# Kernel tuning notes

Hardware: AMD Instinct MI355X
Metric: run time of the kernel (lower is better)

## Reference

```python
import jax, jax.numpy as jnp
import numpy as np

D_MODEL = 1024
NUM_HEADS = 16
GROUPS = 4
HEADS_PER_GROUP = NUM_HEADS // GROUPS
D_K = D_MODEL // NUM_HEADS
B, S = 2, 2048


def setup_inputs() -> dict:
    key = jax.random.key(0)
    ks = jax.random.split(key, 10)
    sc = 0.02
    return {
        "x": jax.random.normal(ks[0], (B, S, D_MODEL), dtype=jnp.float32),
        "W_Q": jax.random.normal(ks[1], (D_MODEL, D_MODEL), dtype=jnp.float32) * sc,
        "b_Q": jnp.zeros((D_MODEL,), dtype=jnp.float32),
        "W_K": jax.random.normal(ks[2], (GROUPS, D_MODEL, D_K), dtype=jnp.float32) * sc,
        "b_K": jnp.zeros((GROUPS, D_K), dtype=jnp.float32),
        "W_V": jax.random.normal(ks[3], (GROUPS, D_MODEL, D_K), dtype=jnp.float32) * sc,
        "b_V": jnp.zeros((GROUPS, D_K), dtype=jnp.float32),
        "W_O": jax.random.normal(ks[4], (D_MODEL, D_MODEL), dtype=jnp.float32) * sc,
        "b_O": jnp.zeros((D_MODEL,), dtype=jnp.float32),
    }


def reference(x, W_Q, b_Q, W_K, b_K, W_V, b_V, W_O, b_O):
    b, s, _ = x.shape
    # Q: [b, s, d_model] -> [b, groups, heads_per_group, s, d_k]
    Q = (x @ W_Q + b_Q).reshape(b, s, NUM_HEADS, D_K).transpose(0, 2, 1, 3)
    Q = Q.reshape(b, GROUPS, HEADS_PER_GROUP, s, D_K)
    # Shared K/V per group: [b, groups, s, d_k]
    K = jnp.einsum('bsd,gdk->bgsk', x, W_K) + b_K[None, :, None, :]
    V = jnp.einsum('bsd,gdk->bgsk', x, W_V) + b_V[None, :, None, :]
    # scores: [b, groups, heads_per_group, s, s]
    scores = jnp.einsum('bghsk,bgtk->bghst', Q, K) / jnp.sqrt(jnp.float32(D_K))
    attn = jax.nn.softmax(scores, axis=-1)
    # context: [b, groups, heads_per_group, s, d_k] -> [b, s, d_model]
    ctx = jnp.einsum('bghst,bgtk->bghsk', attn, V)
    ctx = ctx.reshape(b, NUM_HEADS, s, D_K).transpose(0, 2, 1, 3).reshape(b, s, D_MODEL)
    return ctx @ W_O + b_O
```

## Files before the change

kernel.cpp:

```cpp
#include <hip/hip_runtime.h>
#include <cstdint>
#include <cstddef>

typedef short bf16x8 __attribute__((ext_vector_type(8)));
typedef float f32x4 __attribute__((ext_vector_type(4)));

#define DM 1024
#define NHEADS 16
#define NGROUPS 4
#define DK 64
#define BATCH 2
#define SEQ 2048
#define MROWS 4096

#define QB_ELEMS   ((size_t)BATCH*NHEADS*SEQ*DK)
#define KB_ELEMS   ((size_t)BATCH*NGROUPS*SEQ*DK)
#define VT_ELEMS   KB_ELEMS
#define XC_ELEMS   ((size_t)MROWS*DM)
#define WQKV_ELEMS ((size_t)1536*DM)
#define WO_ELEMS   ((size_t)DM*DM)

__device__ __forceinline__ ushort f2bf(float f) {
    union { float f; uint32_t u; } a; a.f = f;
    uint32_t u = a.u;
    return (ushort)((u + 0x7FFFu + ((u >> 16) & 1u)) >> 16);
}
__device__ __forceinline__ ushort f2bf_rh(float f) {
    union { float f; uint32_t u; } a; a.f = f;
    return (ushort)((a.u + 0x8000u) >> 16);
}

__device__ __forceinline__ void gll16(const void* g, void* l) {
    __builtin_amdgcn_global_load_lds((const __attribute__((address_space(1))) void*)g,
                                     (__attribute__((address_space(3))) void*)l, 16, 0, 0);
}

__global__ __launch_bounds__(256) void gqa_prep_kernel(
        const float* __restrict__ x,
        const float* __restrict__ WQ, const float* __restrict__ WK,
        const float* __restrict__ WV, const float* __restrict__ WO,
        const float* __restrict__ bQ, const float* __restrict__ bK,
        const float* __restrict__ bV,
        ushort* __restrict__ xbf, ushort* __restrict__ WqkvT,
        ushort* __restrict__ WoT, float* __restrict__ bcat)
{
    __shared__ float tl[64][65];
    const int bid = blockIdx.x, tid = threadIdx.x;
    if (bid < 640) {
        const float* src; ushort* dst; int src_ld; int r0, c0;
        if (bid < 256) {
            src = WQ; src_ld = 1024; dst = WqkvT;
            r0 = (bid >> 4) * 64; c0 = (bid & 15) * 64;
        } else if (bid < 512) {
            int t = bid - 256;
            src = WO; src_ld = 1024; dst = WoT;
            r0 = (t >> 4) * 64; c0 = (t & 15) * 64;
        } else if (bid < 576) {
            int t = bid - 512; int g = t >> 4;
            src = WK + (size_t)g * 1024 * 64; src_ld = 64;
            dst = WqkvT + (size_t)(1024 + g * 64) * 1024;
            r0 = (t & 15) * 64; c0 = 0;
        } else {
            int t = bid - 576; int g = t >> 4;
            src = WV + (size_t)g * 1024 * 64; src_ld = 64;
            dst = WqkvT + (size_t)(1280 + g * 64) * 1024;
            r0 = (t & 15) * 64; c0 = 0;
        }
        const int rr = tid >> 4, cc = (tid & 15) * 4;
#pragma unroll
        for (int p = 0; p < 4; p++) {
            int r = rr + p * 16;
            float4 v = *(const float4*)(src + (size_t)(r0 + r) * src_ld + c0 + cc);
            tl[cc + 0][r] = v.x; tl[cc + 1][r] = v.y;
            tl[cc + 2][r] = v.z; tl[cc + 3][r] = v.w;
        }
        __syncthreads();
#pragma unroll
        for (int p = 0; p < 4; p++) {
            int c = rr + p * 16;
            ushort4 o;
            o.x = f2bf(tl[c][cc + 0]); o.y = f2bf(tl[c][cc + 1]);
            o.z = f2bf(tl[c][cc + 2]); o.w = f2bf(tl[c][cc + 3]);
            *(ushort4*)(dst + (size_t)(c0 + c) * 1024 + r0 + cc) = o;
        }
    } else if (bid < 896) {
        int cid = bid - 640;
        const float* xs = x + (size_t)cid * 16384;
        ushort* xd = xbf + (size_t)cid * 16384;
#pragma unroll
        for (int p = 0; p < 16; p++) {
            float4 v = *(const float4*)(xs + p * 1024 + tid * 4);
            ushort4 o = { f2bf(v.x), f2bf(v.y), f2bf(v.z), f2bf(v.w) };
            *(ushort4*)(xd + p * 1024 + tid * 4) = o;
        }
    } else {
        for (int i = tid; i < 1536; i += 256) {
            float v = (i < 1024) ? bQ[i] : (i < 1280 ? bK[i - 1024] : bV[i - 1280]);
            bcat[i] = v;
        }
    }
}

template<bool QKV_EPI>
__global__ __launch_bounds__(256, 2) void gqa_gemm_kernel(
        const ushort* __restrict__ A, const ushort* __restrict__ BT,
        const float* __restrict__ bias, float* __restrict__ outF,
        ushort* __restrict__ Qb, ushort* __restrict__ Kb, ushort* __restrict__ Vtg)
{
    __shared__ ushort As[2][128 * 32];
    __shared__ ushort Bs[2][64 * 32];
    const int tid = threadIdx.x;
    const int bm = blockIdx.x, bn = blockIdx.y;
    const int wave = tid >> 6, lane = tid & 63;
    const int wm = (wave & 1) * 64, wn = (wave >> 1) * 32;
    const int lr = lane & 15, lq = lane >> 4;

    const int sa0 = wave * 128 + lane;
    const int sa1 = sa0 + 64;
    const int sb0 = wave * 64 + lane;
    const ushort* srcA0 = A  + (size_t)(bm * 128 + (sa0 >> 2)) * 1024 + (sa0 & 3) * 8;
    const ushort* srcA1 = A  + (size_t)(bm * 128 + (sa1 >> 2)) * 1024 + (sa1 & 3) * 8;
    const ushort* srcB0 = BT + (size_t)(bn * 64  + (sb0 >> 2)) * 1024 + (sb0 & 3) * 8;

    f32x4 acc[4][2];
#pragma unroll
    for (int i = 0; i < 4; i++)
#pragma unroll
        for (int j = 0; j < 2; j++) acc[i][j] = (f32x4){0.f, 0.f, 0.f, 0.f};

    gll16(srcA0, &As[0][wave * 1024]);
    gll16(srcA1, &As[0][wave * 1024 + 512]);
    gll16(srcB0, &Bs[0][wave * 512]);

    for (int kt = 0; kt < 32; kt++) {
        __syncthreads();
        if (kt < 31) {
            int buf = (kt + 1) & 1, ko = (kt + 1) * 32;
            gll16(srcA0 + ko, &As[buf][wave * 1024]);
            gll16(srcA1 + ko, &As[buf][wave * 1024 + 512]);
            gll16(srcB0 + ko, &Bs[buf][wave * 512]);
        }
        const ushort* as = As[kt & 1];
        const ushort* bs = Bs[kt & 1];
        bf16x8 af[4], bfr[2];
#pragma unroll
        for (int i = 0; i < 4; i++) af[i]  = *(const bf16x8*)&as[(wm + i * 16 + lr) * 32 + lq * 8];
#pragma unroll
        for (int j = 0; j < 2; j++) bfr[j] = *(const bf16x8*)&bs[(wn + j * 16 + lr) * 32 + lq * 8];
#pragma unroll
        for (int i = 0; i < 4; i++)
#pragma unroll
            for (int j = 0; j < 2; j++)
                acc[i][j] = __builtin_amdgcn_mfma_f32_16x16x32_bf16(af[i], bfr[j], acc[i][j], 0, 0, 0);
    }

#pragma unroll
    for (int i = 0; i < 4; i++) {
        int mg = bm * 128 + wm + i * 16 + lq * 4;
        int b = mg >> 11, s = mg & 2047;
#pragma unroll
        for (int j = 0; j < 2; j++) {
            int cg = bn * 64 + wn + j * 16 + lr;
            float bv = bias[cg];
            if constexpr (QKV_EPI) {
                int d = cg & 63;
                if (cg < 1024) {
                    int h = cg >> 6;
                    ushort* dst = Qb + ((size_t)(b * NHEADS + h) * SEQ + s) * DK + d;
#pragma unroll
                    for (int r = 0; r < 4; r++) dst[r * DK] = f2bf(acc[i][j][r] + bv);
                } else if (cg < 1280) {
                    int g = (cg - 1024) >> 6;
                    ushort* dst = Kb + ((size_t)(b * NGROUPS + g) * SEQ + s) * DK + d;
#pragma unroll
                    for (int r = 0; r < 4; r++) dst[r * DK] = f2bf(acc[i][j][r] + bv);
                } else {
                    int g = (cg - 1280) >> 6;
                    ushort4 pk;
                    pk.x = f2bf(acc[i][j][0] + bv); pk.y = f2bf(acc[i][j][1] + bv);
                    pk.z = f2bf(acc[i][j][2] + bv); pk.w = f2bf(acc[i][j][3] + bv);
                    *(ushort4*)(Vtg + ((size_t)(b * NGROUPS + g) * DK + d) * SEQ + s) = pk;
                }
            } else {
#pragma unroll
                for (int r = 0; r < 4; r++)
                    outF[(size_t)(mg + r) * DM + cg] = acc[i][j][r] + bv;
            }
        }
    }
}

__global__ __launch_bounds__(256, 2) void gqa_attn_kernel(
        const ushort* __restrict__ Qb, const ushort* __restrict__ Kb,
        const ushort* __restrict__ Vtg, ushort* __restrict__ ctx)
{
    __shared__ ushort Ks[2][64 * 64];
    __shared__ ushort Vs[2][64 * 64];
    __shared__ ushort Ps[4][32 * 72];

    const int tid = threadIdx.x, wave = tid >> 6, lane = tid & 63;
    const int lr = lane & 15, lq = lane >> 4;
    const int blk = blockIdx.x;
    const int qt = blk & 15, bh = blk >> 4;
    const int b = bh >> 4, hg = bh & 15, g = hg >> 2;

    const ushort* Qh = Qb  + (size_t)(b * NHEADS  + hg) * SEQ * DK;
    const ushort* Kg = Kb  + (size_t)(b * NGROUPS + g)  * SEQ * DK;
    const ushort* Vg = Vtg + (size_t)(b * NGROUPS + g)  * DK * SEQ;

    const int s0 = qt * 128 + wave * 32;

    bf16x8 qf[2][2];
#pragma unroll
    for (int qs = 0; qs < 2; qs++)
#pragma unroll
        for (int h = 0; h < 2; h++)
            qf[qs][h] = *(const bf16x8*)(Qh + (size_t)(s0 + qs * 16 + lr) * DK + h * 32 + lq * 8);

    const int sl0 = wave * 128 + lane, sl1 = sl0 + 64;
    const int row0 = sl0 >> 3, cb0 = (sl0 & 7) ^ (row0 & 7);
    const int row1 = sl1 >> 3, cb1 = (sl1 & 7) ^ (row1 & 7);
    const ushort* srcK0 = Kg + (size_t)row0 * DK + cb0 * 8;
    const ushort* srcK1 = Kg + (size_t)row1 * DK + cb1 * 8;
    const ushort* srcV0 = Vg + (size_t)row0 * SEQ + cb0 * 8;
    const ushort* srcV1 = Vg + (size_t)row1 * SEQ + cb1 * 8;

    f32x4 of[2][4];
#pragma unroll
    for (int qs = 0; qs < 2; qs++)
#pragma unroll
        for (int j = 0; j < 4; j++) of[qs][j] = (f32x4){0.f, 0.f, 0.f, 0.f};
    float lsum[2][4] = {{0.f,0.f,0.f,0.f},{0.f,0.f,0.f,0.f}};

    const float SCL = 0.125f * 1.44269504f;
    ushort* PsW = &Ps[wave][0];
    const int swz = lr & 7;

    gll16(srcK0, &Ks[0][wave * 1024]);
    gll16(srcK1, &Ks[0][wave * 1024 + 512]);
    gll16(srcV0, &Vs[0][wave * 1024]);
    gll16(srcV1, &Vs[0][wave * 1024 + 512]);

    for (int it = 0; it < 32; it++) {
        __syncthreads();
        if (it < 31) {
            int buf = (it + 1) & 1, t0 = (it + 1) * 64;
            gll16(srcK0 + (size_t)t0 * DK, &Ks[buf][wave * 1024]);
            gll16(srcK1 + (size_t)t0 * DK, &Ks[buf][wave * 1024 + 512]);
            gll16(srcV0 + t0, &Vs[buf][wave * 1024]);
            gll16(srcV1 + t0, &Vs[buf][wave * 1024 + 512]);
        }
        const ushort* ks = Ks[it & 1];
        const ushort* vs = Vs[it & 1];

        bf16x8 kf[4][2];
#pragma unroll
        for (int nt = 0; nt < 4; nt++)
#pragma unroll
            for (int h = 0; h < 2; h++)
                kf[nt][h] = *(const bf16x8*)&ks[((nt * 16 + lr) * 8 + ((h * 4 + lq) ^ swz)) * 8];

        f32x4 sc[2][4];
#pragma unroll
        for (int qs = 0; qs < 2; qs++)
#pragma unroll
            for (int nt = 0; nt < 4; nt++) {
                f32x4 s = (f32x4){0.f, 0.f, 0.f, 0.f};
                s = __builtin_amdgcn_mfma_f32_16x16x32_bf16(qf[qs][0], kf[nt][0], s, 0, 0, 0);
                s = __builtin_amdgcn_mfma_f32_16x16x32_bf16(qf[qs][1], kf[nt][1], s, 0, 0, 0);
                sc[qs][nt] = s;
            }

#pragma unroll
        for (int qs = 0; qs < 2; qs++)
#pragma unroll
            for (int nt = 0; nt < 4; nt++)
#pragma unroll
                for (int r = 0; r < 4; r++) {
                    float p = __builtin_amdgcn_exp2f(sc[qs][nt][r] * SCL);
                    lsum[qs][r] += p;
                    PsW[(qs * 16 + lq * 4 + r) * 72 + nt * 16 + lr] = f2bf_rh(p);
                }
        asm volatile("s_waitcnt lgkmcnt(0)" ::: "memory");

        bf16x8 af[2][2], vf[4][2];
#pragma unroll
        for (int qs = 0; qs < 2; qs++)
#pragma unroll
            for (int kh = 0; kh < 2; kh++)
                af[qs][kh] = *(const bf16x8*)&PsW[(qs * 16 + lr) * 72 + kh * 32 + lq * 8];
#pragma unroll
        for (int j = 0; j < 4; j++)
#pragma unroll
            for (int kh = 0; kh < 2; kh++)
                vf[j][kh] = *(const bf16x8*)&vs[((j * 16 + lr) * 8 + ((kh * 4 + lq) ^ swz)) * 8];

#pragma unroll
        for (int qs = 0; qs < 2; qs++)
#pragma unroll
            for (int j = 0; j < 4; j++) {
                of[qs][j] = __builtin_amdgcn_mfma_f32_16x16x32_bf16(af[qs][0], vf[j][0], of[qs][j], 0, 0, 0);
                of[qs][j] = __builtin_amdgcn_mfma_f32_16x16x32_bf16(af[qs][1], vf[j][1], of[qs][j], 0, 0, 0);
            }
    }

    float inv[2][4];
#pragma unroll
    for (int qs = 0; qs < 2; qs++)
#pragma unroll
        for (int r = 0; r < 4; r++) {
            float v = lsum[qs][r];
            v += __shfl_xor(v, 1);
            v += __shfl_xor(v, 2);
            v += __shfl_xor(v, 4);
            v += __shfl_xor(v, 8);
            inv[qs][r] = 1.0f / v;
        }
    ushort* cb = ctx + (size_t)b * SEQ * DM;
#pragma unroll
    for (int qs = 0; qs < 2; qs++)
#pragma unroll
        for (int j = 0; j < 4; j++)
#pragma unroll
            for (int r = 0; r < 4; r++) {
                int s = s0 + qs * 16 + lq * 4 + r;
                cb[(size_t)s * DM + hg * 64 + j * 16 + lr] = f2bf(of[qs][j][r] * inv[qs][r]);
            }
}

extern "C" void kernel_launch(void* const* d_in, const int* in_sizes, int n_in,
                              void* d_out, int out_size, void* d_ws, size_t ws_size,
                              hipStream_t stream) {
    const float* x  = (const float*)d_in[0];
    const float* WQ = (const float*)d_in[1];
    const float* bQ = (const float*)d_in[2];
    const float* WK = (const float*)d_in[3];
    const float* bK = (const float*)d_in[4];
    const float* WV = (const float*)d_in[5];
    const float* bV = (const float*)d_in[6];
    const float* WO = (const float*)d_in[7];
    const float* bO = (const float*)d_in[8];

    ushort* Qb    = (ushort*)d_ws;
    ushort* Kb    = Qb + QB_ELEMS;
    ushort* Vtg   = Kb + KB_ELEMS;
    ushort* xc    = Vtg + VT_ELEMS;
    ushort* WqkvT = xc + XC_ELEMS;
    ushort* WoT   = WqkvT + WQKV_ELEMS;
    float*  bcat  = (float*)(WoT + WO_ELEMS);

    gqa_prep_kernel<<<897, 256, 0, stream>>>(x, WQ, WK, WV, WO, bQ, bK, bV,
                                             xc, WqkvT, WoT, bcat);
    gqa_gemm_kernel<true><<<dim3(32, 24), 256, 0, stream>>>(
        xc, WqkvT, bcat, nullptr, Qb, Kb, Vtg);
    gqa_attn_kernel<<<512, 256, 0, stream>>>(Qb, Kb, Vtg, xc);
    gqa_gemm_kernel<false><<<dim3(32, 16), 256, 0, stream>>>(
        xc, WoT, bO, (float*)d_out, nullptr, nullptr, nullptr);
}
```

Baseline: 185.7 us.

## Enlarge GEMM tiles and keep attention probabilities in registers via transposed MFMA

The GEMM moves from 128x64x32 tiles to 128x128x64 tiles with an XOR-swizzled LDS layout, which doubles per-wave MFMA work per load and halves the grid. The attention kernel swaps MFMA operand order so the score output already sits in the layout needed for the PV product. That lets P stay in registers and drops the LDS round trip and its waitcnt. V is written in a permuted column order to match, attention blocks shrink to 2 waves with twice as many blocks, and context stores become vectorized. The risks are higher register and LDS pressure from the bigger GEMM tiles, fewer GEMM blocks to fill the GPU, and correctness hinging on the V permutation matching the register layout of P.

```diff
diff --git a/kernel.cpp b/kernel.cpp
--- a/kernel.cpp
+++ b/kernel.cpp
@@ -107,51 +107,66 @@
         const float* __restrict__ bias, float* __restrict__ outF,
         ushort* __restrict__ Qb, ushort* __restrict__ Kb, ushort* __restrict__ Vtg)
 {
-    __shared__ ushort As[2][128 * 32];
-    __shared__ ushort Bs[2][64 * 32];
+    __shared__ ushort As[2][128 * 64];
+    __shared__ ushort Bs[2][128 * 64];
     const int tid = threadIdx.x;
     const int bm = blockIdx.x, bn = blockIdx.y;
     const int wave = tid >> 6, lane = tid & 63;
-    const int wm = (wave & 1) * 64, wn = (wave >> 1) * 32;
+    const int wm = (wave & 1) * 64, wn = (wave >> 1) * 64;
     const int lr = lane & 15, lq = lane >> 4;
-
-    const int sa0 = wave * 128 + lane;
-    const int sa1 = sa0 + 64;
-    const int sb0 = wave * 64 + lane;
-    const ushort* srcA0 = A  + (size_t)(bm * 128 + (sa0 >> 2)) * 1024 + (sa0 & 3) * 8;
-    const ushort* srcA1 = A  + (size_t)(bm * 128 + (sa1 >> 2)) * 1024 + (sa1 & 3) * 8;
-    const ushort* srcB0 = BT + (size_t)(bn * 64  + (sb0 >> 2)) * 1024 + (sb0 & 3) * 8;
-
-    f32x4 acc[4][2];
+    const int swz = lr & 7;
+
+    const int cb = (lane & 7) ^ (lane >> 3);
+    const ushort* srcA[4]; const ushort* srcB[4]; int dstOff[4];
+#pragma unroll
+    for (int seg = 0; seg < 4; seg++) {
+        int row = seg * 32 + wave * 8 + (lane >> 3);
+        srcA[seg] = A  + (size_t)(bm * 128 + row) * 1024 + cb * 8;
+        srcB[seg] = BT + (size_t)(bn * 128 + row) * 1024 + cb * 8;
+        dstOff[seg] = seg * 2048 + wave * 512;
+    }
+
+    f32x4 acc[4][4];
 #pragma unroll
     for (int i = 0; i < 4; i++)
 #pragma unroll
-        for (int j = 0; j < 2; j++) acc[i][j] = (f32x4){0.f, 0.f, 0.f, 0.f};
-
-    gll16(srcA0, &As[0][wave * 1024]);
-    gll16(srcA1, &As[0][wave * 1024 + 512]);
-    gll16(srcB0, &Bs[0][wave * 512]);
-
-    for (int kt = 0; kt < 32; kt++) {
+        for (int j = 0; j < 4; j++) acc[i][j] = (f32x4){0.f, 0.f, 0.f, 0.f};
+
+#pragma unroll
+    for (int seg = 0; seg < 4; seg++) {
+        gll16(srcA[seg], &As[0][dstOff[seg]]);
+        gll16(srcB[seg], &Bs[0][dstOff[seg]]);
+    }
+
+    for (int kt = 0; kt < 16; kt++) {
         __syncthreads();
-        if (kt < 31) {
-            int buf = (kt + 1) & 1, ko = (kt + 1) * 32;
-            gll16(srcA0 + ko, &As[buf][wave * 1024]);
-            gll16(srcA1 + ko, &As[buf][wave * 1024 + 512]);
-            gll16(srcB0 + ko, &Bs[buf][wave * 512]);
+        if (kt < 15) {
+            int buf = (kt + 1) & 1, ko = (kt + 1) * 64;
+#pragma unroll
+            for (int seg = 0; seg < 4; seg++) {
+                gll16(srcA[seg] + ko, &As[buf][dstOff[seg]]);
+                gll16(srcB[seg] + ko, &Bs[buf][dstOff[seg]]);
+            }
         }
         const ushort* as = As[kt & 1];
         const ushort* bs = Bs[kt & 1];
-        bf16x8 af[4], bfr[2];
-#pragma unroll
-        for (int i = 0; i < 4; i++) af[i]  = *(const bf16x8*)&as[(wm + i * 16 + lr) * 32 + lq * 8];
-#pragma unroll
-        for (int j = 0; j < 2; j++) bfr[j] = *(const bf16x8*)&bs[(wn + j * 16 + lr) * 32 + lq * 8];
-#pragma unroll
-        for (int i = 0; i < 4; i++)
-#pragma unroll
-            for (int j = 0; j < 2; j++)
-                acc[i][j] = __builtin_amdgcn_mfma_f32_16x16x32_bf16(af[i], bfr[j], acc[i][j], 0, 0, 0);
+        bf16x8 af[2][4], bfr[2][4];
+#pragma unroll
+        for (int kh = 0; kh < 2; kh++) {
+#pragma unroll
+            for (int i = 0; i < 4; i++)
+                af[kh][i] = *(const bf16x8*)&as[(wm + i * 16 + lr) * 64 + (((kh * 4 + lq) ^ swz)) * 8];
+#pragma unroll
+            for (int j = 0; j < 4; j++)
+                bfr[kh][j] = *(const bf16x8*)&bs[(wn + j * 16 + lr) * 64 + (((kh * 4 + lq) ^ swz)) * 8];
+        }
+#pragma unroll
+        for (int kh = 0; kh < 2; kh++)
+#pragma unroll
+            for (int i = 0; i < 4; i++)
+#pragma unroll
+                for (int j = 0; j < 4; j++)
+                    acc[i][j] = __builtin_amdgcn_mfma_f32_16x16x32_bf16(af[kh][i], bfr[kh][j], acc[i][j], 0, 0, 0);
     }
 
 #pragma unroll
@@ -159,8 +174,8 @@
         int mg = bm * 128 + wm + i * 16 + lq * 4;
         int b = mg >> 11, s = mg & 2047;
 #pragma unroll
-        for (int j = 0; j < 2; j++) {
-            int cg = bn * 64 + wn + j * 16 + lr;
+        for (int j = 0; j < 4; j++) {
+            int cg = bn * 128 + wn + j * 16 + lr;
             float bv = bias[cg];
             if constexpr (QKV_EPI) {
                 int d = cg & 63;
@@ -176,10 +191,12 @@
                     for (int r = 0; r < 4; r++) dst[r * DK] = f2bf(acc[i][j][r] + bv);
                 } else {
                     int g = (cg - 1280) >> 6;
+                    int s4 = s >> 2, kg = s4 & 7;
+                    int col = ((s4 >> 3) << 5) + (((((kg & 3) << 1) | (kg >> 2))) << 2);
                     ushort4 pk;
                     pk.x = f2bf(acc[i][j][0] + bv); pk.y = f2bf(acc[i][j][1] + bv);
                     pk.z = f2bf(acc[i][j][2] + bv); pk.w = f2bf(acc[i][j][3] + bv);
-                    *(ushort4*)(Vtg + ((size_t)(b * NGROUPS + g) * DK + d) * SEQ + s) = pk;
+                    *(ushort4*)(Vtg + ((size_t)(b * NGROUPS + g) * DK + d) * SEQ + col) = pk;
                 }
             } else {
 #pragma unroll
@@ -190,25 +207,25 @@
     }
 }
 
-__global__ __launch_bounds__(256, 2) void gqa_attn_kernel(
+__global__ __launch_bounds__(128, 2) void gqa_attn_kernel(
         const ushort* __restrict__ Qb, const ushort* __restrict__ Kb,
         const ushort* __restrict__ Vtg, ushort* __restrict__ ctx)
 {
     __shared__ ushort Ks[2][64 * 64];
     __shared__ ushort Vs[2][64 * 64];
-    __shared__ ushort Ps[4][32 * 72];
 
     const int tid = threadIdx.x, wave = tid >> 6, lane = tid & 63;
     const int lr = lane & 15, lq = lane >> 4;
+    const int swz = lr & 7;
     const int blk = blockIdx.x;
-    const int qt = blk & 15, bh = blk >> 4;
+    const int qt = blk & 31, bh = blk >> 5;
     const int b = bh >> 4, hg = bh & 15, g = hg >> 2;
 
     const ushort* Qh = Qb  + (size_t)(b * NHEADS  + hg) * SEQ * DK;
     const ushort* Kg = Kb  + (size_t)(b * NGROUPS + g)  * SEQ * DK;
     const ushort* Vg = Vtg + (size_t)(b * NGROUPS + g)  * DK * SEQ;
 
-    const int s0 = qt * 128 + wave * 32;
+    const int s0 = qt * 64 + wave * 32;
 
     bf16x8 qf[2][2];
 #pragma unroll
@@ -217,38 +234,40 @@
         for (int h = 0; h < 2; h++)
             qf[qs][h] = *(const bf16x8*)(Qh + (size_t)(s0 + qs * 16 + lr) * DK + h * 32 + lq * 8);
 
-    const int sl0 = wave * 128 + lane, sl1 = sl0 + 64;
-    const int row0 = sl0 >> 3, cb0 = (sl0 & 7) ^ (row0 & 7);
-    const int row1 = sl1 >> 3, cb1 = (sl1 & 7) ^ (row1 & 7);
-    const ushort* srcK0 = Kg + (size_t)row0 * DK + cb0 * 8;
-    const ushort* srcK1 = Kg + (size_t)row1 * DK + cb1 * 8;
-    const ushort* srcV0 = Vg + (size_t)row0 * SEQ + cb0 * 8;
-    const ushort* srcV1 = Vg + (size_t)row1 * SEQ + cb1 * 8;
+    const int cb = (lane & 7) ^ (lane >> 3);
+    const ushort* srcK[4]; const ushort* srcV[4]; int dstOff[4];
+#pragma unroll
+    for (int seg = 0; seg < 4; seg++) {
+        int row = wave * 32 + seg * 8 + (lane >> 3);
+        srcK[seg] = Kg + (size_t)row * DK + cb * 8;
+        srcV[seg] = Vg + (size_t)row * SEQ + cb * 8;
+        dstOff[seg] = wave * 2048 + seg * 512;
+    }
 
     f32x4 of[2][4];
 #pragma unroll
     for (int qs = 0; qs < 2; qs++)
 #pragma unroll
         for (int j = 0; j < 4; j++) of[qs][j] = (f32x4){0.f, 0.f, 0.f, 0.f};
-    float lsum[2][4] = {{0.f,0.f,0.f,0.f},{0.f,0.f,0.f,0.f}};
+    float lsum[2] = {0.f, 0.f};
 
     const float SCL = 0.125f * 1.44269504f;
-    ushort* PsW = &Ps[wave][0];
-    const int swz = lr & 7;
-
-    gll16(srcK0, &Ks[0][wave * 1024]);
-    gll16(srcK1, &Ks[0][wave * 1024 + 512]);
-    gll16(srcV0, &Vs[0][wave * 1024]);
-    gll16(srcV1, &Vs[0][wave * 1024 + 512]);
+
+#pragma unroll
+    for (int seg = 0; seg < 4; seg++) {
+        gll16(srcK[seg], &Ks[0][dstOff[seg]]);
+        gll16(srcV[seg], &Vs[0][dstOff[seg]]);
+    }
 
     for (int it = 0; it < 32; it++) {
         __syncthreads();
         if (it < 31) {
             int buf = (it + 1) & 1, t0 = (it + 1) * 64;
-            gll16(srcK0 + (size_t)t0 * DK, &Ks[buf][wave * 1024]);
-            gll16(srcK1 + (size_t)t0 * DK, &Ks[buf][wave * 1024 + 512]);
-            gll16(srcV0 + t0, &Vs[buf][wave * 1024]);
-            gll16(srcV1 + t0, &Vs[buf][wave * 1024 + 512]);
+#pragma unroll
+            for (int seg = 0; seg < 4; seg++) {
+                gll16(srcK[seg] + (size_t)t0 * DK, &Ks[buf][dstOff[seg]]);
+                gll16(srcV[seg] + t0, &Vs[buf][dstOff[seg]]);
+            }
         }
         const ushort* ks = Ks[it & 1];
         const ushort* vs = Vs[it & 1];
@@ -266,11 +285,12 @@
 #pragma unroll
             for (int nt = 0; nt < 4; nt++) {
                 f32x4 s = (f32x4){0.f, 0.f, 0.f, 0.f};
-                s = __builtin_amdgcn_mfma_f32_16x16x32_bf16(qf[qs][0], kf[nt][0], s, 0, 0, 0);
-                s = __builtin_amdgcn_mfma_f32_16x16x32_bf16(qf[qs][1], kf[nt][1], s, 0, 0, 0);
+                s = __builtin_amdgcn_mfma_f32_16x16x32_bf16(kf[nt][0], qf[qs][0], s, 0, 0, 0);
+                s = __builtin_amdgcn_mfma_f32_16x16x32_bf16(kf[nt][1], qf[qs][1], s, 0, 0, 0);
                 sc[qs][nt] = s;
             }
 
+        union { bf16x8 v; ushort u[8]; } pf[2][2];
 #pragma unroll
         for (int qs = 0; qs < 2; qs++)
 #pragma unroll
@@ -278,17 +298,11 @@
 #pragma unroll
                 for (int r = 0; r < 4; r++) {
                     float p = __builtin_amdgcn_exp2f(sc[qs][nt][r] * SCL);
-                    lsum[qs][r] += p;
-                    PsW[(qs * 16 + lq * 4 + r) * 72 + nt * 16 + lr] = f2bf_rh(p);
+                    lsum[qs] += p;
+                    pf[qs][nt >> 1].u[(nt & 1) * 4 + r] = f2bf_rh(p);
                 }
-        asm volatile("s_waitcnt lgkmcnt(0)" ::: "memory");
-
-        bf16x8 af[2][2], vf[4][2];
-#pragma unroll
-        for (int qs = 0; qs < 2; qs++)
-#pragma unroll
-            for (int kh = 0; kh < 2; kh++)
-                af[qs][kh] = *(const bf16x8*)&PsW[(qs * 16 + lr) * 72 + kh * 32 + lq * 8];
+
+        bf16x8 vf[4][2];
 #pragma unroll
         for (int j = 0; j < 4; j++)
 #pragma unroll
@@ -299,33 +313,33 @@
         for (int qs = 0; qs < 2; qs++)
 #pragma unroll
             for (int j = 0; j < 4; j++) {
-                of[qs][j] = __builtin_amdgcn_mfma_f32_16x16x32_bf16(af[qs][0], vf[j][0], of[qs][j], 0, 0, 0);
-                of[qs][j] = __builtin_amdgcn_mfma_f32_16x16x32_bf16(af[qs][1], vf[j][1], of[qs][j], 0, 0, 0);
-            }
-    }
-
-    float inv[2][4];
-#pragma unroll
-    for (int qs = 0; qs < 2; qs++)
-#pragma unroll
-        for (int r = 0; r < 4; r++) {
-            float v = lsum[qs][r];
-            v += __shfl_xor(v, 1);
-            v += __shfl_xor(v, 2);
-            v += __shfl_xor(v, 4);
-            v += __shfl_xor(v, 8);
-            inv[qs][r] = 1.0f / v;
-        }
-    ushort* cb = ctx + (size_t)b * SEQ * DM;
-#pragma unroll
-    for (int qs = 0; qs < 2; qs++)
-#pragma unroll
-        for (int j = 0; j < 4; j++)
-#pragma unroll
-            for (int r = 0; r < 4; r++) {
-                int s = s0 + qs * 16 + lq * 4 + r;
-                cb[(size_t)s * DM + hg * 64 + j * 16 + lr] = f2bf(of[qs][j][r] * inv[qs][r]);
-            }
+                of[qs][j] = __builtin_amdgcn_mfma_f32_16x16x32_bf16(vf[j][0], pf[qs][0].v, of[qs][j], 0, 0, 0);
+                of[qs][j] = __builtin_amdgcn_mfma_f32_16x16x32_bf16(vf[j][1], pf[qs][1].v, of[qs][j], 0, 0, 0);
+            }
+    }
+
+    float inv[2];
+#pragma unroll
+    for (int qs = 0; qs < 2; qs++) {
+        float v = lsum[qs];
+        v += __shfl_xor(v, 16);
+        v += __shfl_xor(v, 32);
+        inv[qs] = 1.0f / v;
+    }
+    ushort* cbp = ctx + (size_t)b * SEQ * DM;
+#pragma unroll
+    for (int qs = 0; qs < 2; qs++) {
+        int s = s0 + qs * 16 + lr;
+#pragma unroll
+        for (int j = 0; j < 4; j++) {
+            ushort4 o;
+            o.x = f2bf(of[qs][j][0] * inv[qs]);
+            o.y = f2bf(of[qs][j][1] * inv[qs]);
+            o.z = f2bf(of[qs][j][2] * inv[qs]);
+            o.w = f2bf(of[qs][j][3] * inv[qs]);
+            *(ushort4*)(cbp + (size_t)s * DM + hg * 64 + j * 16 + lq * 4) = o;
+        }
+    }
 }
 
 extern "C" void kernel_launch(void* const* d_in, const int* in_sizes, int n_in,
@@ -351,9 +365,9 @@
 
     gqa_prep_kernel<<<897, 256, 0, stream>>>(x, WQ, WK, WV, WO, bQ, bK, bV,
                                              xc, WqkvT, WoT, bcat);
-    gqa_gemm_kernel<true><<<dim3(32, 24), 256, 0, stream>>>(
+    gqa_gemm_kernel<true><<<dim3(32, 12), 256, 0, stream>>>(
         xc, WqkvT, bcat, nullptr, Qb, Kb, Vtg);
-    gqa_attn_kernel<<<512, 256, 0, stream>>>(Qb, Kb, Vtg, xc);
-    gqa_gemm_kernel<false><<<dim3(32, 16), 256, 0, stream>>>(
+    gqa_attn_kernel<<<1024, 128, 0, stream>>>(Qb, Kb, Vtg, xc);
+    gqa_gemm_kernel<false><<<dim3(32, 8), 256, 0, stream>>>(
         xc, WoT, bO, (float*)d_out, nullptr, nullptr, nullptr);
 }
```

Measured after the change: 185.1 us. No clear change (-0.3%).
